# Kernel tuning notes

Measured on AMD Instinct MI355X. Metric: run time of the kernel, lower is better.

The kernel has to match this reference:

```python
import jax, jax.numpy as jnp
import numpy as np

# ---- config (matches init_kwargs + VMamba/MambaIR SS2D defaults) ----
B, LEN, C, H, W = 2, 3, 64, 64, 64
N_STATE = 16           # d_state
D_INNER = 2 * C        # expand=2
DT_RANK = C // 16      # ceil(d_model/16)
K = 4                  # 4 scan directions
EPS = 1e-5


def _ln_last(x, g, b):
    m = x.mean(-1, keepdims=True)
    v = x.var(-1, keepdims=True)
    return (x - m) * jax.lax.rsqrt(v + EPS) * g + b


def _instance_ln(x):
    # kalman.utils.layer_norm: normalize each sample over (C,H,W), no affine
    m = x.mean(axis=(1, 2, 3), keepdims=True)
    v = x.var(axis=(1, 2, 3), keepdims=True)
    return (x - m) * jax.lax.rsqrt(v + EPS)


def _gn(x, g, b):
    # GroupNorm with num_groups=1 on NCHW
    m = x.mean(axis=(1, 2, 3), keepdims=True)
    v = x.var(axis=(1, 2, 3), keepdims=True)
    return (x - m) * jax.lax.rsqrt(v + EPS) * g[None, :, None, None] + b[None, :, None, None]


def _conv2d(x, w, b, groups=1):
    y = jax.lax.conv_general_dilated(x, w, (1, 1), 'SAME',
            dimension_numbers=('NCHW', 'OIHW', 'NCHW'), feature_group_count=groups)
    return y + b[None, :, None, None]


def _selective_scan(xs, dts, Bs, Cs, A, Ds, dt_bias):
    # xs, dts: (Bt,K,D,L); Bs, Cs: (Bt,K,N,L); A: (K,D,N); Ds, dt_bias: (K,D)
    delta = jax.nn.softplus(dts + dt_bias[None, :, :, None])
    u_t = jnp.moveaxis(xs, -1, 0)      # (L,Bt,K,D)
    d_t = jnp.moveaxis(delta, -1, 0)
    B_t = jnp.moveaxis(Bs, -1, 0)      # (L,Bt,K,N)
    C_t = jnp.moveaxis(Cs, -1, 0)
    h0 = jnp.zeros((xs.shape[0], K, xs.shape[2], A.shape[-1]), xs.dtype)

    def step(h, inp):
        u, d, Bv, Cv = inp
        dA = jnp.exp(d[..., None] * A)                                  # (Bt,K,D,N)
        h = dA * h + d[..., None] * Bv[:, :, None, :] * u[..., None]
        y = jnp.einsum('bkdn,bkn->bkd', h, Cv)
        return h, y

    _, ys = jax.lax.scan(step, h0, (u_t, d_t, B_t, C_t))
    ys = jnp.moveaxis(ys, 0, -1)                                        # (Bt,K,D,L)
    return ys + xs * Ds[None, :, :, None]


def _ss2d(x, in_proj_w, dwconv_w, dwconv_b, x_proj_w, dt_proj_w, dt_proj_b,
          A_logs, Ds, out_norm_g, out_norm_b, out_proj_w):
    Bt, Hh, Ww, Cc = x.shape
    L = Hh * Ww
    xz = x @ in_proj_w.T                               # (Bt,H,W,2*Di)
    xx, z = jnp.split(xz, 2, axis=-1)
    xx = jnp.transpose(xx, (0, 3, 1, 2))               # (Bt,Di,H,W)
    xx = jax.nn.silu(_conv2d(xx, dwconv_w, dwconv_b, groups=D_INNER))
    hw = xx.reshape(Bt, D_INNER, L)
    wh = jnp.transpose(xx, (0, 1, 3, 2)).reshape(Bt, D_INNER, L)
    xs = jnp.stack([hw, wh, hw[..., ::-1], wh[..., ::-1]], axis=1)      # (Bt,4,Di,L)
    x_dbl = jnp.einsum('bkdl,kcd->bkcl', xs, x_proj_w)
    dts = jnp.einsum('bkrl,kdr->bkdl', x_dbl[:, :, :DT_RANK], dt_proj_w)
    Bs = x_dbl[:, :, DT_RANK:DT_RANK + N_STATE]
    Cs = x_dbl[:, :, DT_RANK + N_STATE:]
    A = -jnp.exp(A_logs)                               # (K,Di,N)
    out_y = _selective_scan(xs, dts, Bs, Cs, A, Ds, dt_proj_b)
    inv = out_y[:, 2:4, :, ::-1]

    def wh2hw(y):
        return jnp.transpose(y.reshape(Bt, D_INNER, Ww, Hh), (0, 1, 3, 2)).reshape(Bt, D_INNER, L)

    y = out_y[:, 0] + inv[:, 0] + wh2hw(out_y[:, 1]) + wh2hw(inv[:, 1])
    y = jnp.transpose(y.reshape(Bt, D_INNER, Hh, Ww), (0, 2, 3, 1))
    y = _ln_last(y, out_norm_g, out_norm_b)
    y = y * jax.nn.silu(z)
    return y @ out_proj_w.T


def setup_inputs() -> dict:
    key = jax.random.key(0)
    ks = jax.random.split(key, 16)
    rn = lambda k, s, sc=0.05: jax.random.normal(k, s, jnp.float32) * sc
    inp = {}
    inp['image_sequence'] = jax.random.normal(ks[0], (B, LEN, C, H, W), jnp.float32)
    inp['difficult_zone'] = jax.random.normal(ks[1], (B, C, H, W), jnp.float32)
    inp['sigma'] = jax.random.uniform(ks[2], (B, C, H, W), jnp.float32)
    inp['gn1_g'] = jnp.ones((3 * C,)); inp['gn1_b'] = jnp.zeros((3 * C,))
    inp['conv1_w'] = rn(ks[3], (C, 3 * C, 3, 3)); inp['conv1_b'] = jnp.zeros((C,))
    inp['gn2_g'] = jnp.ones((C,)); inp['gn2_b'] = jnp.zeros((C,))
    inp['conv2_w'] = rn(ks[4], (C, C, 3, 3)); inp['conv2_b'] = jnp.zeros((C,))
    inp['skip_w'] = rn(ks[5], (C, 3 * C, 1, 1)); inp['skip_b'] = jnp.zeros((C,))
    inp['ln1_g'] = jnp.ones((C,)); inp['ln1_b'] = jnp.zeros((C,))
    inp['ln2_g'] = jnp.ones((C,)); inp['ln2_b'] = jnp.zeros((C,))
    inp['in_proj_w'] = rn(ks[6], (2 * D_INNER, C))
    inp['dwconv_w'] = rn(ks[7], (D_INNER, 1, 3, 3)); inp['dwconv_b'] = jnp.zeros((D_INNER,))
    inp['x_proj_w'] = rn(ks[8], (K, DT_RANK + 2 * N_STATE, D_INNER))
    inp['dt_proj_w'] = rn(ks[9], (K, D_INNER, DT_RANK), 0.2)
    inp['dt_proj_b'] = rn(ks[10], (K, D_INNER), 0.1)
    inp['A_logs'] = jnp.log(jnp.broadcast_to(jnp.arange(1, N_STATE + 1, dtype=jnp.float32), (K, D_INNER, N_STATE)))
    inp['Ds'] = jnp.ones((K, D_INNER))
    inp['out_norm_g'] = jnp.ones((D_INNER,)); inp['out_norm_b'] = jnp.zeros((D_INNER,))
    inp['out_proj_w'] = rn(ks[11], (C, D_INNER))
    inp['fc1_w'] = rn(ks[12], (C, C)); inp['fc1_b'] = jnp.zeros((C,))
    inp['fc2_w'] = rn(ks[13], (C, C)); inp['fc2_b'] = jnp.zeros((C,))
    return inp


def reference(image_sequence, difficult_zone, sigma,
              gn1_g, gn1_b, conv1_w, conv1_b, gn2_g, gn2_b, conv2_w, conv2_b, skip_w, skip_b,
              ln1_g, ln1_b, ln2_g, ln2_b,
              in_proj_w, dwconv_w, dwconv_b, x_proj_w, dt_proj_w, dt_proj_b,
              A_logs, Ds, out_norm_g, out_norm_b, out_proj_w,
              fc1_w, fc1_b, fc2_w, fc2_b):
    Bsz, Lf, Cc, Hh, Ww = image_sequence.shape
    # per-frame layer_norm; frames are independent so fold them into batch
    img = _instance_ln(image_sequence.reshape(Bsz * Lf, Cc, Hh, Ww)).reshape(Bsz, Lf, Cc, Hh, Ww)
    dz = jnp.broadcast_to(difficult_zone[:, None], (Bsz, Lf, Cc, Hh, Ww))
    sg = jnp.broadcast_to(sigma[:, None], (Bsz, Lf, Cc, Hh, Ww))
    x = jnp.concatenate([dz, img, sg], axis=2).reshape(Bsz * Lf, 3 * Cc, Hh, Ww)
    # ConvolutionalResBlock (GN -> SiLU -> conv, x2, + 1x1 skip)
    h = _conv2d(jax.nn.silu(_gn(x, gn1_g, gn1_b)), conv1_w, conv1_b)
    h = _conv2d(jax.nn.silu(_gn(h, gn2_g, gn2_b)), conv2_w, conv2_b)
    x = h + _conv2d(x, skip_w, skip_b)
    # VSSBlock (pre-norm): x + SS2D(LN(x)); x + Mlp(LN(x))
    x = jnp.transpose(x, (0, 2, 3, 1))                 # NHWC
    x = x + _ss2d(_ln_last(x, ln1_g, ln1_b), in_proj_w, dwconv_w, dwconv_b,
                  x_proj_w, dt_proj_w, dt_proj_b, A_logs, Ds,
                  out_norm_g, out_norm_b, out_proj_w)
    xm = _ln_last(x, ln2_g, ln2_b)
    x = x + (jax.nn.gelu(xm @ fc1_w.T + fc1_b) @ fc2_w.T + fc2_b)
    x = jnp.transpose(x, (0, 3, 1, 2)).reshape(Bsz, Lf, Cc, Hh, Ww)
    return x
```

## Files before the change

kernel.cpp:

```cpp
#include <hip/hip_runtime.h>
#include <hip/hip_bf16.h>

typedef unsigned short ushortT;
typedef short short8v __attribute__((ext_vector_type(8)));
typedef float float4v __attribute__((ext_vector_type(4)));

#define NBL 6
#define NC 64
#define NC3 192
#define NHW 4096
#define NDI 128
#define NNS 16
#define NDR 4
#define NK 4
#define NL 4096
#define NCH 128
#define SCLEN 32
#define NSTATE 49152

static const size_t F_XCAT  = 0;
static const size_t F_ACT1  = 4718592;
static const size_t F_H1    = 9437184;
static const size_t F_ACT2  = 11010048;
static const size_t F_H2    = 12582912;
static const size_t F_XRES  = 14155776;
static const size_t F_XXIN  = 15728640;
static const size_t F_Z     = 18874368;
static const size_t F_XXC   = 22020096;
static const size_t F_XDBL  = 25165824;
static const size_t F_YS    = 28704768;
static const size_t F_YCOMB = 41287680;
static const size_t F_X1    = 44433408;
static const size_t F_X2    = 46006272;
static const size_t F_STATS = 47579136;
static const size_t F_TOTAL = 47579184;

__device__ __forceinline__ float wred64(float v) {
#pragma unroll
  for (int m = 32; m; m >>= 1) v += __shfl_xor(v, m, 64);
  return v;
}

__device__ __forceinline__ float silu(float v) {
  return v / (1.f + __expf(-v));
}

__device__ __forceinline__ ushortT f2bf(float f) {
  unsigned int u = __builtin_bit_cast(unsigned int, f);
  unsigned int r = (u + 0x7FFFu + ((u >> 16) & 1u)) >> 16;
  return (ushortT)r;
}

__device__ __forceinline__ int map_pos(int k, int l) {
  if (k == 0) return l;
  if (k == 1) return ((l & 63) << 6) | (l >> 6);
  if (k == 2) return 4095 - l;
  int lp = 4095 - l;
  return ((lp & 63) << 6) | (lp >> 6);
}

__device__ __forceinline__ float softplus_fast(float a) {
  float t = exp2f(a * 1.44269504f);
  float r = 0.69314718f * __log2f(1.f + t);
  return (a > 20.f) ? a : r;
}

__device__ __forceinline__ void pow_tree(float E1, float4v& e0, float4v& e1,
                                         float4v& e2, float4v& e3) {
  float E2 = E1 * E1, E3 = E2 * E1, E4 = E2 * E2;
  float E5 = E4 * E1, E6 = E4 * E2, E7 = E4 * E3, E8 = E4 * E4;
  e0[0] = E1; e0[1] = E2; e0[2] = E3; e0[3] = E4;
  e1[0] = E5; e1[1] = E6; e1[2] = E7; e1[3] = E8;
  e2[0] = E8 * E1; e2[1] = E8 * E2; e2[2] = E8 * E3; e2[3] = E8 * E4;
  e3[0] = E8 * E5; e3[1] = E8 * E6; e3[2] = E8 * E7; e3[3] = E8 * E8;
}

__global__ __launch_bounds__(256) void wtrans_kernel(const float* __restrict__ src,
                                                     float* __restrict__ dst, int O, int C) {
  int id = blockIdx.x * 256 + threadIdx.x;
  if (id >= O * C) return;
  int c = id / O, o = id % O;
  dst[id] = src[o * C + c];
}

__global__ __launch_bounds__(256) void stats1_kernel(const float* __restrict__ in, int n,
                                                     double* __restrict__ part) {
  int bi = blockIdx.x;
  int s = bi >> 5, j = bi & 31;
  int slice = n >> 5;
  const float4* p = (const float4*)(in + (size_t)s * n + (size_t)j * slice);
  int n4 = slice >> 2;
  double dsum = 0.0, dsq = 0.0;
  for (int i = threadIdx.x; i < n4; i += 256) {
    float4 v = p[i];
    dsum += (double)((v.x + v.y) + (v.z + v.w));
    dsq += (double)v.x * v.x + (double)v.y * v.y + (double)v.z * v.z + (double)v.w * v.w;
  }
  __shared__ double s1[256], s2[256];
  s1[threadIdx.x] = dsum; s2[threadIdx.x] = dsq;
  __syncthreads();
  for (int off = 128; off; off >>= 1) {
    if (threadIdx.x < off) { s1[threadIdx.x] += s1[threadIdx.x + off]; s2[threadIdx.x] += s2[threadIdx.x + off]; }
    __syncthreads();
  }
  if (threadIdx.x == 0) { part[2 * bi] = s1[0]; part[2 * bi + 1] = s2[0]; }
}

__global__ __launch_bounds__(64) void stats2_kernel(const double* __restrict__ part, int n,
                                                    float* __restrict__ mean_out,
                                                    float* __restrict__ rstd_out) {
  int s = blockIdx.x;
  int lane = threadIdx.x;
  double sum = 0.0, sq = 0.0;
  if (lane < 32) { sum = part[2 * (s * 32 + lane)]; sq = part[2 * (s * 32 + lane) + 1]; }
#pragma unroll
  for (int m = 16; m; m >>= 1) { sum += __shfl_xor(sum, m, 64); sq += __shfl_xor(sq, m, 64); }
  if (lane == 0) {
    double mean = sum / n;
    double var = sq / n - mean * mean;
    mean_out[s] = (float)mean;
    rstd_out[s] = (float)(1.0 / sqrt(var + 1e-5));
  }
}

__global__ __launch_bounds__(256) void build_xcat_kernel(const float* __restrict__ img,
                                                         const float* __restrict__ dz,
                                                         const float* __restrict__ sg,
                                                         const float* __restrict__ stats,
                                                         float* __restrict__ xcat) {
  size_t gid = (size_t)blockIdx.x * 256 + threadIdx.x;
  int p = gid & 4095;
  size_t r = gid >> 12;
  int ch = (int)(r % NC3);
  int bl = (int)(r / NC3);
  int b = bl / 3;
  float v;
  if (ch < 64) {
    v = dz[((size_t)b * NC + ch) * NHW + p];
  } else if (ch < 128) {
    float m = stats[bl], rs = stats[8 + bl];
    v = (img[((size_t)bl * NC + (ch - 64)) * NHW + p] - m) * rs;
  } else {
    v = sg[((size_t)b * NC + (ch - 128)) * NHW + p];
  }
  xcat[gid] = v;
}

template <int CCH>
__global__ __launch_bounds__(256) void gnsilu_t_kernel(const float* __restrict__ in,
                                                       const float* __restrict__ g,
                                                       const float* __restrict__ b,
                                                       const float* __restrict__ stats,
                                                       ushortT* __restrict__ outb) {
  int bi = blockIdx.x;
  int bl = bi >> 6, h = bi & 63;
  __shared__ ushortT tile[CCH][66];
  float m = stats[bl], rs = stats[8 + bl];
  int t = threadIdx.x;
  for (int idx = t; idx < CCH * 64; idx += 256) {
    int ch = idx >> 6, w = idx & 63;
    float v = in[(((size_t)bl * CCH + ch) << 12) + (h << 6) + w];
    v = (v - m) * rs * g[ch] + b[ch];
    v = silu(v);
    tile[ch][w] = f2bf(v);
  }
  __syncthreads();
  constexpr int C8 = CCH / 8;
  for (int idx = t; idx < 64 * C8; idx += 256) {
    int w = idx / C8, c8 = idx % C8;
    short8v v;
#pragma unroll
    for (int j = 0; j < 8; ++j) v[j] = (short)tile[c8 * 8 + j][w];
    *(short8v*)&outb[(size_t)(bl * 4096 + h * 64 + w) * CCH + c8 * 8] = v;
  }
}

__global__ __launch_bounds__(256) void wprep_kernel(const float* __restrict__ w,
                                                    ushortT* __restrict__ out,
                                                    int CIN, int KT) {
  int id = blockIdx.x * 256 + threadIdx.x;
  int j = id & 7;
  int lane = (id >> 3) & 63;
  int nt = (id >> 9) & 3;
  int rest = id >> 11;
  int kt = rest % KT;
  int tap = rest / KT;
  int oc = nt * 16 + (lane & 15);
  int ic = kt * 32 + ((lane >> 4) << 3) + j;
  int r = tap / 3, s = tap % 3;
  out[id] = f2bf(w[(((size_t)oc * CIN + ic) * 3 + r) * 3 + s]);
}

template <int CIN>
__global__ __launch_bounds__(256) void conv_mfma_kernel(const ushortT* __restrict__ actb,
                                                        const ushortT* __restrict__ wb,
                                                        const float* __restrict__ bias,
                                                        float* __restrict__ out) {
  constexpr int KT = CIN / 32;
  constexpr int STRIDE = CIN + 8;
  constexpr int C8 = CIN / 8;
  int bi = blockIdx.x;
  int nh = bi & 1;
  int h = (bi >> 1) & 63;
  int bl = bi >> 7;
  int t = threadIdx.x;
  int wv = t >> 6, lane = t & 63;
  __shared__ ushortT lds[66 * STRIDE];
  float4v acc0 = {0.f, 0.f, 0.f, 0.f};
  float4v acc1 = {0.f, 0.f, 0.f, 0.f};
  int lrow = lane & 15;
  int lk = (lane >> 4) << 3;
  for (int dy = 0; dy < 3; ++dy) {
    int hh = h + dy - 1;
    bool valid = (hh >= 0) && (hh < 64);
    int hc = valid ? hh : 0;
    if (dy) __syncthreads();
    const ushortT* src = actb + (size_t)(bl * 4096 + hc * 64) * CIN;
    for (int idx = t; idx < 64 * C8; idx += 256) {
      int w = idx / C8, c8 = idx % C8;
      short8v v = {0, 0, 0, 0, 0, 0, 0, 0};
      if (valid) v = *(const short8v*)&src[(size_t)w * CIN + c8 * 8];
      *(short8v*)&lds[(w + 1) * STRIDE + c8 * 8] = v;
    }
    if (t < 2 * C8) {
      int which = t / C8, c8 = t % C8;
      short8v z = {0, 0, 0, 0, 0, 0, 0, 0};
      *(short8v*)&lds[(which ? 65 : 0) * STRIDE + c8 * 8] = z;
    }
    __syncthreads();
    for (int dx = 0; dx < 3; ++dx) {
      int tap = dy * 3 + dx;
      int wl = (wv << 4) + lrow + dx;
#pragma unroll
      for (int kt = 0; kt < KT; ++kt) {
        short8v a = *(const short8v*)&lds[wl * STRIDE + kt * 32 + lk];
        const ushortT* wp = wb + ((size_t)(((tap * KT + kt) * 4 + (nh << 1)) * 64 + lane) << 3);
        short8v b0 = *(const short8v*)&wp[0];
        short8v b1 = *(const short8v*)&wp[512];
        acc0 = __builtin_amdgcn_mfma_f32_16x16x32_bf16(a, b0, acc0, 0, 0, 0);
        acc1 = __builtin_amdgcn_mfma_f32_16x16x32_bf16(a, b1, acc1, 0, 0, 0);
      }
    }
  }
  int oc0 = (nh << 5) + lrow;
  int oc1 = oc0 + 16;
  int w0 = (wv << 4) + ((lane >> 4) << 2);
  float bv0 = bias[oc0], bv1 = bias[oc1];
  float4 o0 = make_float4(acc0[0] + bv0, acc0[1] + bv0, acc0[2] + bv0, acc0[3] + bv0);
  float4 o1 = make_float4(acc1[0] + bv1, acc1[1] + bv1, acc1[2] + bv1, acc1[3] + bv1);
  *(float4*)&out[(((size_t)bl * 64 + oc0) << 12) + (h << 6) + w0] = o0;
  *(float4*)&out[(((size_t)bl * 64 + oc1) << 12) + (h << 6) + w0] = o1;
}

__global__ __launch_bounds__(256) void skip_kernel(const float* __restrict__ xcat,
                                                   const float* __restrict__ h2,
                                                   const float* __restrict__ skwt,
                                                   const float* __restrict__ skb,
                                                   float* __restrict__ xres) {
  int bi = blockIdx.x;
  int bl = bi >> 6, h = bi & 63;
  int t = threadIdx.x;
  int oc = t & 63, w0 = (t >> 6) << 4;
  __shared__ float lds[64][64];
  float acc[16];
#pragma unroll
  for (int i = 0; i < 16; ++i) acc[i] = 0.f;
  for (int cc = 0; cc < 3; ++cc) {
    __syncthreads();
    for (int idx = t; idx < 4096; idx += 256) {
      int ch = idx >> 6, w = idx & 63;
      lds[ch][w] = xcat[(((size_t)bl * NC3 + cc * 64 + ch) << 12) + (h << 6) + w];
    }
    __syncthreads();
    for (int ch = 0; ch < 64; ++ch) {
      float wv = skwt[((cc << 6) + ch) * 64 + oc];
#pragma unroll
      for (int i = 0; i < 16; ++i) acc[i] += wv * lds[ch][w0 + i];
    }
  }
  float bv = skb[oc];
  int p0 = (h << 6) + w0;
#pragma unroll
  for (int i = 0; i < 16; ++i) {
    float hv = h2[(((size_t)bl * 64 + oc) << 12) + p0 + i];
    xres[((size_t)bl * NHW + p0 + i) * 64 + oc] = acc[i] + bv + hv;
  }
}

__global__ __launch_bounds__(256) void inproj_kernel(const float* __restrict__ xres,
                                                     const float* __restrict__ g,
                                                     const float* __restrict__ b,
                                                     const float* __restrict__ wt,
                                                     float* __restrict__ xxin,
                                                     float* __restrict__ z) {
  int wv = threadIdx.x >> 6, lane = threadIdx.x & 63;
  size_t pi0 = (size_t)blockIdx.x << 4;
  __shared__ float xb[64][16];
  float gv = g[lane], bv = b[lane];
#pragma unroll
  for (int j = 0; j < 4; ++j) {
    int p = (wv << 2) + j;
    float x = xres[(pi0 + p) * 64 + lane];
    float s = wred64(x);
    float s2 = wred64(x * x);
    float m = s * (1.f / 64), var = s2 * (1.f / 64) - m * m;
    float rstd = rsqrtf(var + 1e-5f);
    xb[lane][p] = (x - m) * rstd * gv + bv;
  }
  __syncthreads();
  int oc = (wv << 6) + lane;
  float4v a0 = {0.f, 0.f, 0.f, 0.f}, a1 = a0, a2 = a0, a3 = a0;
  for (int c = 0; c < 64; ++c) {
    float w = wt[(c << 8) + oc];
    const float4v* xr = (const float4v*)&xb[c][0];
    a0 += w * xr[0];
    a1 += w * xr[1];
    a2 += w * xr[2];
    a3 += w * xr[3];
  }
  float acc[16];
  *(float4v*)&acc[0] = a0;
  *(float4v*)&acc[4] = a1;
  *(float4v*)&acc[8] = a2;
  *(float4v*)&acc[12] = a3;
  float* dst = (oc < 128) ? xxin : z;
  int oco = (oc < 128) ? oc : (oc - 128);
#pragma unroll
  for (int p = 0; p < 16; ++p) dst[((pi0 + p) << 7) + oco] = acc[p];
}

__global__ __launch_bounds__(256) void dwconv_kernel(const float* __restrict__ xx,
                                                     const float* __restrict__ w,
                                                     const float* __restrict__ b,
                                                     float* __restrict__ out) {
  size_t gid = (size_t)blockIdx.x * 256 + threadIdx.x;
  int d = gid & 127;
  size_t pi = gid >> 7;
  int p = (int)(pi & 4095);
  int bl = (int)(pi >> 12);
  int h = p >> 6, wq = p & 63;
  float acc = b[d];
  const float* wr = w + d * 9;
#pragma unroll
  for (int dy = -1; dy <= 1; ++dy) {
    int hh = h + dy;
    if (hh < 0 || hh >= 64) continue;
#pragma unroll
    for (int dx = -1; dx <= 1; ++dx) {
      int ww = wq + dx;
      if (ww < 0 || ww >= 64) continue;
      acc += wr[(dy + 1) * 3 + (dx + 1)] * xx[(((size_t)bl << 12) + (hh << 6) + ww) * 128 + d];
    }
  }
  out[pi * 128 + d] = silu(acc);
}

__global__ __launch_bounds__(256) void xdbl_kernel(const float* __restrict__ xxc,
                                                   const float* __restrict__ xpw,
                                                   float* __restrict__ xdbl) {
  int bi = blockIdx.x;
  int lt = bi & 63;
  int korder = (bi >> 6) & 1;
  int bl = bi >> 7;
  int lbase = lt << 6;
  __shared__ float xs[64 * 128];
  int t = threadIdx.x;
#pragma unroll
  for (int it = 0; it < 8; ++it) {
    int idx = it * 256 + t;
    int i = idx >> 5, d4 = idx & 31;
    int l = lbase + i;
    int pos = korder ? (((l & 63) << 6) | (l >> 6)) : l;
    float4 v = *(const float4*)&xxc[((size_t)bl * NHW + pos) * 128 + (d4 << 2)];
    int slot = d4 ^ (i & 7);
    *(float4*)&xs[i * 128 + (slot << 2)] = v;
  }
  __syncthreads();
  int wv = __builtin_amdgcn_readfirstlane(t >> 6);
  int lane = t & 63;
  int k_w = korder + ((wv >= 2) ? 2 : 0);
  int c0 = (wv & 1) * 18;
  float acc[18];
#pragma unroll
  for (int j = 0; j < 18; ++j) acc[j] = 0.f;
  const float* wbase = xpw + (size_t)(k_w * 36 + c0) * 128;
  for (int d4 = 0; d4 < 32; ++d4) {
    int slot = d4 ^ (lane & 7);
    float4 x4 = *(const float4*)&xs[lane * 128 + (slot << 2)];
#pragma unroll
    for (int j = 0; j < 18; ++j) {
      float4 w4 = *(const float4*)&wbase[j * 128 + (d4 << 2)];
      acc[j] += w4.x * x4.x + w4.y * x4.y + w4.z * x4.z + w4.w * x4.w;
    }
  }
  int lout = (k_w < 2) ? (lbase + lane) : (4095 - lbase - lane);
  size_t obase = ((size_t)(bl * 4 + k_w) * 36 + c0) * (size_t)NL + lout;
#pragma unroll
  for (int j = 0; j < 18; ++j)
    xdbl[obase + (size_t)j * NL] = acc[j];
}

__global__ __launch_bounds__(128) void scan_pass1_kernel(const float* __restrict__ xdbl,
                                                         const float* __restrict__ xxc,
                                                         const float* __restrict__ dtw,
                                                         const float* __restrict__ dtb,
                                                         const float* __restrict__ Alog,
                                                         float* __restrict__ chunkP,
                                                         float* __restrict__ chunkH) {
  int bi = blockIdx.x;
  int chunk = bi & (NCH - 1);
  int bk = bi >> 7;
  int k = bk & 3, bl = bk >> 2;
  int d = threadIdx.x;
  float4 wv = *(const float4*)(dtw + (size_t)(((k << 7) + d) << 2));
  float bias = dtb[(k << 7) + d];
  const float* ar = Alog + (size_t)(((k << 7) + d) << 4);
  float a1v = -__expf(ar[0]) * 1.44269504f;
  bool geom = true;
#pragma unroll
  for (int n = 1; n < 16; ++n) {
    float an = -__expf(ar[n]) * 1.44269504f;
    geom = geom && (fabsf(an - (float)(n + 1) * a1v) <= 1e-3f * fabsf((float)(n + 1) * a1v) + 1e-6f);
  }
  __shared__ float xd[SCLEN][20];
  int l0 = chunk << 5;
  for (int idx = threadIdx.x; idx < 20 * SCLEN; idx += 128) {
    int c = idx >> 5, li = idx & 31;
    xd[li][c] = xdbl[((size_t)bk * 36 + c) * (size_t)NL + l0 + li];
  }
  __syncthreads();
  const float* uB = xxc + ((size_t)bl << 19) + d;
  float4v h0 = {0.f, 0.f, 0.f, 0.f}, h1 = h0, h2 = h0, h3 = h0;
  float sdt = 0.f;
  float u_nxt = uB[(size_t)map_pos(k, l0) << 7];
  if (geom) {
    for (int li = 0; li < SCLEN; ++li) {
      float u = u_nxt;
      int nl = (li < SCLEN - 1) ? (li + 1) : (SCLEN - 1);
      u_nxt = uB[(size_t)map_pos(k, l0 + nl) << 7];
      const float4v* row = (const float4v*)&xd[li][0];
      float4v q0 = row[0];
      float accq = bias + wv.x * q0[0] + wv.y * q0[1] + wv.z * q0[2] + wv.w * q0[3];
      float dt = softplus_fast(accq);
      float dtu = dt * u;
      sdt += dt;
      float4v b0 = row[1], b1 = row[2], b2 = row[3], b3 = row[4];
      float4v e0, e1, e2, e3;
      pow_tree(exp2f(a1v * dt), e0, e1, e2, e3);
      h0 = e0 * h0 + dtu * b0;
      h1 = e1 * h1 + dtu * b1;
      h2 = e2 * h2 + dtu * b2;
      h3 = e3 * h3 + dtu * b3;
    }
  } else {
    float4v a0v, a1q, a2q, a3q;
#pragma unroll
    for (int j = 0; j < 4; ++j) {
      a0v[j] = -__expf(ar[j]) * 1.44269504f;
      a1q[j] = -__expf(ar[4 + j]) * 1.44269504f;
      a2q[j] = -__expf(ar[8 + j]) * 1.44269504f;
      a3q[j] = -__expf(ar[12 + j]) * 1.44269504f;
    }
    for (int li = 0; li < SCLEN; ++li) {
      float u = u_nxt;
      int nl = (li < SCLEN - 1) ? (li + 1) : (SCLEN - 1);
      u_nxt = uB[(size_t)map_pos(k, l0 + nl) << 7];
      const float4v* row = (const float4v*)&xd[li][0];
      float4v q0 = row[0];
      float accq = bias + wv.x * q0[0] + wv.y * q0[1] + wv.z * q0[2] + wv.w * q0[3];
      float dt = softplus_fast(accq);
      float dtu = dt * u;
      sdt += dt;
      float4v b0 = row[1], b1 = row[2], b2 = row[3], b3 = row[4];
      float4v e0, e1, e2, e3;
#pragma unroll
      for (int j = 0; j < 4; ++j) {
        e0[j] = exp2f(a0v[j] * dt);
        e1[j] = exp2f(a1q[j] * dt);
        e2[j] = exp2f(a2q[j] * dt);
        e3[j] = exp2f(a3q[j] * dt);
      }
      h0 = e0 * h0 + dtu * b0;
      h1 = e1 * h1 + dtu * b1;
      h2 = e2 * h2 + dtu * b2;
      h3 = e3 * h3 + dtu * b3;
    }
  }
  size_t base = (size_t)chunk * NSTATE + (((size_t)bk << 7) + (size_t)d) * 16;
  float4v p0, p1, p2, p3;
  if (geom) {
    pow_tree(exp2f(a1v * sdt), p0, p1, p2, p3);
  } else {
#pragma unroll
    for (int j = 0; j < 4; ++j) {
      p0[j] = exp2f(-__expf(ar[j]) * 1.44269504f * sdt);
      p1[j] = exp2f(-__expf(ar[4 + j]) * 1.44269504f * sdt);
      p2[j] = exp2f(-__expf(ar[8 + j]) * 1.44269504f * sdt);
      p3[j] = exp2f(-__expf(ar[12 + j]) * 1.44269504f * sdt);
    }
  }
  *(float4v*)&chunkP[base + 0] = p0;
  *(float4v*)&chunkP[base + 4] = p1;
  *(float4v*)&chunkP[base + 8] = p2;
  *(float4v*)&chunkP[base + 12] = p3;
  *(float4v*)&chunkH[base + 0] = h0;
  *(float4v*)&chunkH[base + 4] = h1;
  *(float4v*)&chunkH[base + 8] = h2;
  *(float4v*)&chunkH[base + 12] = h3;
}

__global__ __launch_bounds__(256) void scan_pass2_kernel(const float* __restrict__ chunkP,
                                                         const float* __restrict__ chunkH,
                                                         float* __restrict__ chunkHS) {
  size_t state = (size_t)blockIdx.x * 256 + threadIdx.x;
  float h = 0.f;
#pragma unroll 4
  for (int j = 0; j < NCH; ++j) {
    size_t idx = (size_t)j * NSTATE + state;
    chunkHS[idx] = h;
    h = chunkP[idx] * h + chunkH[idx];
  }
}

__global__ __launch_bounds__(128) void scan_pass3_kernel(const float* __restrict__ xdbl,
                                                         const float* __restrict__ xxc,
                                                         const float* __restrict__ dtw,
                                                         const float* __restrict__ dtb,
                                                         const float* __restrict__ Alog,
                                                         const float* __restrict__ chunkHS,
                                                         float* __restrict__ ys) {
  int bi = blockIdx.x;
  int chunk = bi & (NCH - 1);
  int bk = bi >> 7;
  int k = bk & 3, bl = bk >> 2;
  int d = threadIdx.x;
  float4 wv = *(const float4*)(dtw + (size_t)(((k << 7) + d) << 2));
  float bias = dtb[(k << 7) + d];
  const float* ar = Alog + (size_t)(((k << 7) + d) << 4);
  float a1v = -__expf(ar[0]) * 1.44269504f;
  bool geom = true;
#pragma unroll
  for (int n = 1; n < 16; ++n) {
    float an = -__expf(ar[n]) * 1.44269504f;
    geom = geom && (fabsf(an - (float)(n + 1) * a1v) <= 1e-3f * fabsf((float)(n + 1) * a1v) + 1e-6f);
  }
  __shared__ float xd[SCLEN][36];
  int l0 = chunk << 5;
  for (int idx = threadIdx.x; idx < 36 * SCLEN; idx += 128) {
    int c = idx >> 5, li = idx & 31;
    xd[li][c] = xdbl[((size_t)bk * 36 + c) * (size_t)NL + l0 + li];
  }
  __syncthreads();
  const float* uB = xxc + ((size_t)bl << 19) + d;
  float* yB = ys + ((size_t)bk << 19) + d;
  size_t base = (size_t)chunk * NSTATE + (((size_t)bk << 7) + (size_t)d) * 16;
  float4v h0 = *(const float4v*)&chunkHS[base + 0];
  float4v h1 = *(const float4v*)&chunkHS[base + 4];
  float4v h2 = *(const float4v*)&chunkHS[base + 8];
  float4v h3 = *(const float4v*)&chunkHS[base + 12];
  float u_nxt = uB[(size_t)map_pos(k, l0) << 7];
  if (geom) {
    for (int li = 0; li < SCLEN; ++li) {
      float u = u_nxt;
      int nl = (li < SCLEN - 1) ? (li + 1) : (SCLEN - 1);
      u_nxt = uB[(size_t)map_pos(k, l0 + nl) << 7];
      const float4v* row = (const float4v*)&xd[li][0];
      float4v q0 = row[0];
      float accq = bias + wv.x * q0[0] + wv.y * q0[1] + wv.z * q0[2] + wv.w * q0[3];
      float dt = softplus_fast(accq);
      float dtu = dt * u;
      float4v b0 = row[1], b1 = row[2], b2 = row[3], b3 = row[4];
      float4v c0 = row[5], c1 = row[6], c2 = row[7], c3 = row[8];
      float4v e0, e1, e2, e3;
      pow_tree(exp2f(a1v * dt), e0, e1, e2, e3);
      h0 = e0 * h0 + dtu * b0;
      h1 = e1 * h1 + dtu * b1;
      h2 = e2 * h2 + dtu * b2;
      h3 = e3 * h3 + dtu * b3;
      float4v sy = h0 * c0;
      sy += h1 * c1;
      sy += h2 * c2;
      sy += h3 * c3;
      yB[(size_t)(l0 + li) << 7] = (sy[0] + sy[1]) + (sy[2] + sy[3]);
    }
  } else {
    float4v a0v, a1q, a2q, a3q;
#pragma unroll
    for (int j = 0; j < 4; ++j) {
      a0v[j] = -__expf(ar[j]) * 1.44269504f;
      a1q[j] = -__expf(ar[4 + j]) * 1.44269504f;
      a2q[j] = -__expf(ar[8 + j]) * 1.44269504f;
      a3q[j] = -__expf(ar[12 + j]) * 1.44269504f;
    }
    for (int li = 0; li < SCLEN; ++li) {
      float u = u_nxt;
      int nl = (li < SCLEN - 1) ? (li + 1) : (SCLEN - 1);
      u_nxt = uB[(size_t)map_pos(k, l0 + nl) << 7];
      const float4v* row = (const float4v*)&xd[li][0];
      float4v q0 = row[0];
      float accq = bias + wv.x * q0[0] + wv.y * q0[1] + wv.z * q0[2] + wv.w * q0[3];
      float dt = softplus_fast(accq);
      float dtu = dt * u;
      float4v b0 = row[1], b1 = row[2], b2 = row[3], b3 = row[4];
      float4v c0 = row[5], c1 = row[6], c2 = row[7], c3 = row[8];
      float4v e0, e1, e2, e3;
#pragma unroll
      for (int j = 0; j < 4; ++j) {
        e0[j] = exp2f(a0v[j] * dt);
        e1[j] = exp2f(a1q[j] * dt);
        e2[j] = exp2f(a2q[j] * dt);
        e3[j] = exp2f(a3q[j] * dt);
      }
      h0 = e0 * h0 + dtu * b0;
      h1 = e1 * h1 + dtu * b1;
      h2 = e2 * h2 + dtu * b2;
      h3 = e3 * h3 + dtu * b3;
      float4v sy = h0 * c0;
      sy += h1 * c1;
      sy += h2 * c2;
      sy += h3 * c3;
      yB[(size_t)(l0 + li) << 7] = (sy[0] + sy[1]) + (sy[2] + sy[3]);
    }
  }
}

__global__ __launch_bounds__(256) void combine_kernel(const float* __restrict__ ys,
                                                      const float* __restrict__ xxc,
                                                      const float* __restrict__ Ds,
                                                      float* __restrict__ ycomb) {
  size_t gid = (size_t)blockIdx.x * 256 + threadIdx.x;
  int d = gid & 127;
  size_t pi = gid >> 7;
  int p = (int)(pi & 4095);
  int bl = (int)(pi >> 12);
  int h = p >> 6, w = p & 63;
  int l1 = (w << 6) | h;
  size_t base = ((size_t)bl * 4) << 12;
  float v = ys[((base + p) << 7) + d]
          + ys[((base + 4096 + l1) << 7) + d]
          + ys[((base + 2 * 4096 + (4095 - p)) << 7) + d]
          + ys[((base + 3 * 4096 + (4095 - l1)) << 7) + d];
  float ds = Ds[d] + Ds[128 + d] + Ds[256 + d] + Ds[384 + d];
  v += xxc[(pi << 7) + d] * ds;
  ycomb[(pi << 7) + d] = v;
}

__global__ __launch_bounds__(256) void outproj_kernel(const float* __restrict__ ycomb,
                                                      const float* __restrict__ z,
                                                      const float* __restrict__ ong,
                                                      const float* __restrict__ onb,
                                                      const float* __restrict__ opwt,
                                                      const float* __restrict__ xres,
                                                      float* __restrict__ x1) {
  int wv = threadIdx.x >> 6, lane = threadIdx.x & 63;
  size_t pi0 = (size_t)blockIdx.x << 4;
  __shared__ float gb[128][16];
  float og0 = ong[lane], ob0 = onb[lane];
  float og1 = ong[64 + lane], ob1 = onb[64 + lane];
#pragma unroll
  for (int j = 0; j < 4; ++j) {
    int p = (wv << 2) + j;
    size_t pp = pi0 + p;
    float y0 = ycomb[(pp << 7) + lane], y1 = ycomb[(pp << 7) + 64 + lane];
    float s = wred64(y0 + y1);
    float s2 = wred64(y0 * y0 + y1 * y1);
    float m = s * (1.f / 128), var = s2 * (1.f / 128) - m * m;
    float rstd = rsqrtf(var + 1e-5f);
    float z0 = z[(pp << 7) + lane], z1 = z[(pp << 7) + 64 + lane];
    gb[lane][p] = ((y0 - m) * rstd * og0 + ob0) * silu(z0);
    gb[64 + lane][p] = ((y1 - m) * rstd * og1 + ob1) * silu(z1);
  }
  __syncthreads();
  int p0 = wv << 2;
  float4v acc = {0.f, 0.f, 0.f, 0.f};
  for (int c = 0; c < 128; ++c) {
    float w = opwt[(c << 6) + lane];
    acc += w * (*(const float4v*)&gb[c][p0]);
  }
  float accs[4];
  *(float4v*)&accs[0] = acc;
#pragma unroll
  for (int j = 0; j < 4; ++j) {
    size_t pp = pi0 + p0 + j;
    x1[pp * 64 + lane] = xres[pp * 64 + lane] + accs[j];
  }
}

__global__ __launch_bounds__(256) void mlp_kernel(const float* __restrict__ x1,
                                                  const float* __restrict__ g2,
                                                  const float* __restrict__ b2,
                                                  const float* __restrict__ w1t,
                                                  const float* __restrict__ bb1,
                                                  const float* __restrict__ w2t,
                                                  const float* __restrict__ bb2,
                                                  float* __restrict__ x2) {
  int wv = threadIdx.x >> 6, lane = threadIdx.x & 63;
  size_t pi0 = (size_t)blockIdx.x << 4;
  __shared__ float xb[64][16], tb[64][16];
  float gv = g2[lane], bv = b2[lane];
  float xsave[4];
#pragma unroll
  for (int j = 0; j < 4; ++j) {
    int p = (wv << 2) + j;
    float xv = x1[(pi0 + p) * 64 + lane];
    xsave[j] = xv;
    float s = wred64(xv), s2 = wred64(xv * xv);
    float m = s * (1.f / 64), var = s2 * (1.f / 64) - m * m;
    float rstd = rsqrtf(var + 1e-5f);
    xb[lane][p] = (xv - m) * rstd * gv + bv;
  }
  __syncthreads();
  int p0 = wv << 2;
  float bb1v = bb1[lane];
  float4v acc = {bb1v, bb1v, bb1v, bb1v};
  for (int c = 0; c < 64; ++c) {
    float w = w1t[(c << 6) + lane];
    acc += w * (*(const float4v*)&xb[c][p0]);
  }
  float us[4];
  *(float4v*)&us[0] = acc;
#pragma unroll
  for (int j = 0; j < 4; ++j) {
    float u = us[j];
    float tt = tanhf(0.7978845608028654f * (u + 0.044715f * u * u * u));
    tb[lane][p0 + j] = 0.5f * u * (1.f + tt);
  }
  __syncthreads();
  float bb2v = bb2[lane];
  float4v acc2 = {bb2v, bb2v, bb2v, bb2v};
  for (int c = 0; c < 64; ++c) {
    float w = w2t[(c << 6) + lane];
    acc2 += w * (*(const float4v*)&tb[c][p0]);
  }
  float o2[4];
  *(float4v*)&o2[0] = acc2;
#pragma unroll
  for (int j = 0; j < 4; ++j)
    x2[(pi0 + p0 + j) * 64 + lane] = xsave[j] + o2[j];
}

__global__ __launch_bounds__(256) void transpose_out_kernel(const float* __restrict__ x2,
                                                            float* __restrict__ out) {
  int bi = blockIdx.x;
  int pt = bi & 127;
  int ct = (bi >> 7) & 1;
  int bl = bi >> 8;
  __shared__ float lds[32][33];
  int t = threadIdx.x;
  int j = t & 31, i0 = t >> 5;
  int p0 = pt << 5, c0 = ct << 5;
#pragma unroll
  for (int q = 0; q < 4; ++q) {
    int i = i0 + (q << 3);
    lds[i][j] = x2[((size_t)bl * NHW + p0 + i) * 64 + c0 + j];
  }
  __syncthreads();
#pragma unroll
  for (int q = 0; q < 4; ++q) {
    int i = i0 + (q << 3);
    out[((size_t)bl * 64 + c0 + i) * (size_t)NHW + p0 + j] = lds[j][i];
  }
}

extern "C" void kernel_launch(void* const* d_in, const int* in_sizes, int n_in,
                              void* d_out, int out_size, void* d_ws, size_t ws_size,
                              hipStream_t stream) {
  const float* img  = (const float*)d_in[0];
  const float* dz   = (const float*)d_in[1];
  const float* sg   = (const float*)d_in[2];
  const float* gn1g = (const float*)d_in[3];
  const float* gn1b = (const float*)d_in[4];
  const float* c1w  = (const float*)d_in[5];
  const float* c1b  = (const float*)d_in[6];
  const float* gn2g = (const float*)d_in[7];
  const float* gn2b = (const float*)d_in[8];
  const float* c2w  = (const float*)d_in[9];
  const float* c2b  = (const float*)d_in[10];
  const float* skw  = (const float*)d_in[11];
  const float* skb  = (const float*)d_in[12];
  const float* ln1g = (const float*)d_in[13];
  const float* ln1b = (const float*)d_in[14];
  const float* ln2g = (const float*)d_in[15];
  const float* ln2b = (const float*)d_in[16];
  const float* ipw  = (const float*)d_in[17];
  const float* dww  = (const float*)d_in[18];
  const float* dwb  = (const float*)d_in[19];
  const float* xpw  = (const float*)d_in[20];
  const float* dtw  = (const float*)d_in[21];
  const float* dtb  = (const float*)d_in[22];
  const float* Alog = (const float*)d_in[23];
  const float* Dsp  = (const float*)d_in[24];
  const float* ong  = (const float*)d_in[25];
  const float* onb  = (const float*)d_in[26];
  const float* opw  = (const float*)d_in[27];
  const float* f1w  = (const float*)d_in[28];
  const float* f1b  = (const float*)d_in[29];
  const float* f2w  = (const float*)d_in[30];
  const float* f2b  = (const float*)d_in[31];

  float* out = (float*)d_out;
  float* ws = (float*)d_ws;
  if (ws_size < F_TOTAL * sizeof(float)) return;

  float* xcat  = ws + F_XCAT;
  float* h1    = ws + F_H1;
  float* h2    = ws + F_H2;
  float* xres  = ws + F_XRES;
  float* xxin  = ws + F_XXIN;
  float* zbuf  = ws + F_Z;
  float* xxc   = ws + F_XXC;
  float* xdbl  = ws + F_XDBL;
  float* ysb   = ws + F_YS;
  float* ycomb = ws + F_YCOMB;
  float* x1    = ws + F_X1;
  float* x2    = ws + F_X2;
  float* stats = ws + F_STATS;
  ushortT* act1b = (ushortT*)(ws + F_ACT1);
  ushortT* act2b = (ushortT*)(ws + F_ACT2);
  double* part  = (double*)(ws + F_X2);
  ushortT* wb1  = (ushortT*)(ws + F_X2 + 1024);
  ushortT* wb2  = wb1 + 110592;
  float* chunkP  = ws + F_YS;
  float* chunkH  = ws + F_YS + 6291456;
  float* chunkHS = ws + F_XCAT;
  float* wt_sk = ws + F_ACT1;
  float* wt_ip = ws + F_XCAT;
  float* wt_op = ws + F_XXIN;
  float* wt_f1 = ws + F_XXIN + 8192;
  float* wt_f2 = ws + F_XXIN + 12288;

  wprep_kernel<<<432, 256, 0, stream>>>(c1w, wb1, NC3, 6);
  wprep_kernel<<<144, 256, 0, stream>>>(c2w, wb2, NC, 2);
  stats1_kernel<<<NBL * 32, 256, 0, stream>>>(img, NC * NHW, part);
  stats2_kernel<<<NBL, 64, 0, stream>>>(part, NC * NHW, stats + 0, stats + 8);
  build_xcat_kernel<<<18432, 256, 0, stream>>>(img, dz, sg, stats, xcat);
  stats1_kernel<<<NBL * 32, 256, 0, stream>>>(xcat, NC3 * NHW, part);
  stats2_kernel<<<NBL, 64, 0, stream>>>(part, NC3 * NHW, stats + 16, stats + 24);
  gnsilu_t_kernel<NC3><<<NBL * 64, 256, 0, stream>>>(xcat, gn1g, gn1b, stats + 16, act1b);
  conv_mfma_kernel<NC3><<<NBL * 64 * 2, 256, 0, stream>>>(act1b, wb1, c1b, h1);
  wtrans_kernel<<<48, 256, 0, stream>>>(skw, wt_sk, 64, 192);
  stats1_kernel<<<NBL * 32, 256, 0, stream>>>(h1, NC * NHW, part);
  stats2_kernel<<<NBL, 64, 0, stream>>>(part, NC * NHW, stats + 32, stats + 40);
  gnsilu_t_kernel<NC><<<NBL * 64, 256, 0, stream>>>(h1, gn2g, gn2b, stats + 32, act2b);
  conv_mfma_kernel<NC><<<NBL * 64 * 2, 256, 0, stream>>>(act2b, wb2, c2b, h2);
  skip_kernel<<<NBL * 64, 256, 0, stream>>>(xcat, h2, wt_sk, skb, xres);
  wtrans_kernel<<<64, 256, 0, stream>>>(ipw, wt_ip, 256, 64);
  inproj_kernel<<<1536, 256, 0, stream>>>(xres, ln1g, ln1b, wt_ip, xxin, zbuf);
  dwconv_kernel<<<12288, 256, 0, stream>>>(xxin, dww, dwb, xxc);
  wtrans_kernel<<<32, 256, 0, stream>>>(opw, wt_op, 64, 128);
  wtrans_kernel<<<16, 256, 0, stream>>>(f1w, wt_f1, 64, 64);
  wtrans_kernel<<<16, 256, 0, stream>>>(f2w, wt_f2, 64, 64);
  xdbl_kernel<<<NBL * 2 * 64, 256, 0, stream>>>(xxc, xpw, xdbl);
  scan_pass1_kernel<<<24 * NCH, 128, 0, stream>>>(xdbl, xxc, dtw, dtb, Alog, chunkP, chunkH);
  scan_pass2_kernel<<<192, 256, 0, stream>>>(chunkP, chunkH, chunkHS);
  scan_pass3_kernel<<<24 * NCH, 128, 0, stream>>>(xdbl, xxc, dtw, dtb, Alog, chunkHS, ysb);
  combine_kernel<<<12288, 256, 0, stream>>>(ysb, xxc, Dsp, ycomb);
  outproj_kernel<<<1536, 256, 0, stream>>>(ycomb, zbuf, ong, onb, wt_op, xres, x1);
  mlp_kernel<<<1536, 256, 0, stream>>>(x1, ln2g, ln2b, wt_f1, f1b, wt_f2, f2b, x2);
  transpose_out_kernel<<<NBL * 256, 256, 0, stream>>>(x2, out);
}
```

Before: 355.1 us.

## Store per-chunk dt sums instead of decay products and fuse combine into outproj

Scan pass 1 now writes one summed dt per chunk and channel instead of 16 per-state decay factors. Pass 2 recomputes each decay with exp2f from A_log and that sum, which cuts the chunkP write and read traffic. The four-direction combine plus the D skip term moves into the out-projection kernel, removing the ycomb intermediate and one launch. The cost is extra exp work in the serial pass-2 loop, and the 4-way gather now sits inside outproj.

```diff
diff --git a/kernel.cpp b/kernel.cpp
--- a/kernel.cpp
+++ b/kernel.cpp
@@ -405,7 +405,7 @@
                                                          const float* __restrict__ dtw,
                                                          const float* __restrict__ dtb,
                                                          const float* __restrict__ Alog,
-                                                         float* __restrict__ chunkP,
+                                                         float* __restrict__ chunkSdt,
                                                          float* __restrict__ chunkH) {
   int bi = blockIdx.x;
   int chunk = bi & (NCH - 1);
@@ -487,38 +487,26 @@
     }
   }
   size_t base = (size_t)chunk * NSTATE + (((size_t)bk << 7) + (size_t)d) * 16;
-  float4v p0, p1, p2, p3;
-  if (geom) {
-    pow_tree(exp2f(a1v * sdt), p0, p1, p2, p3);
-  } else {
-#pragma unroll
-    for (int j = 0; j < 4; ++j) {
-      p0[j] = exp2f(-__expf(ar[j]) * 1.44269504f * sdt);
-      p1[j] = exp2f(-__expf(ar[4 + j]) * 1.44269504f * sdt);
-      p2[j] = exp2f(-__expf(ar[8 + j]) * 1.44269504f * sdt);
-      p3[j] = exp2f(-__expf(ar[12 + j]) * 1.44269504f * sdt);
-    }
-  }
-  *(float4v*)&chunkP[base + 0] = p0;
-  *(float4v*)&chunkP[base + 4] = p1;
-  *(float4v*)&chunkP[base + 8] = p2;
-  *(float4v*)&chunkP[base + 12] = p3;
+  chunkSdt[(size_t)chunk * 3072 + (bk << 7) + d] = sdt;
   *(float4v*)&chunkH[base + 0] = h0;
   *(float4v*)&chunkH[base + 4] = h1;
   *(float4v*)&chunkH[base + 8] = h2;
   *(float4v*)&chunkH[base + 12] = h3;
 }
 
-__global__ __launch_bounds__(256) void scan_pass2_kernel(const float* __restrict__ chunkP,
+__global__ __launch_bounds__(256) void scan_pass2_kernel(const float* __restrict__ chunkSdt,
                                                          const float* __restrict__ chunkH,
+                                                         const float* __restrict__ Alog,
                                                          float* __restrict__ chunkHS) {
   size_t state = (size_t)blockIdx.x * 256 + threadIdx.x;
+  float an = -__expf(Alog[state & 8191]) * 1.44269504f;
+  int kd = (int)(state >> 4);
   float h = 0.f;
-#pragma unroll 4
   for (int j = 0; j < NCH; ++j) {
     size_t idx = (size_t)j * NSTATE + state;
     chunkHS[idx] = h;
-    h = chunkP[idx] * h + chunkH[idx];
+    float sdt = chunkSdt[(size_t)j * 3072 + kd];
+    h = exp2f(an * sdt) * h + chunkH[idx];
   }
 }
 
@@ -624,28 +612,9 @@
   }
 }
 
-__global__ __launch_bounds__(256) void combine_kernel(const float* __restrict__ ys,
+__global__ __launch_bounds__(256) void outproj_kernel(const float* __restrict__ ys,
                                                       const float* __restrict__ xxc,
                                                       const float* __restrict__ Ds,
-                                                      float* __restrict__ ycomb) {
-  size_t gid = (size_t)blockIdx.x * 256 + threadIdx.x;
-  int d = gid & 127;
-  size_t pi = gid >> 7;
-  int p = (int)(pi & 4095);
-  int bl = (int)(pi >> 12);
-  int h = p >> 6, w = p & 63;
-  int l1 = (w << 6) | h;
-  size_t base = ((size_t)bl * 4) << 12;
-  float v = ys[((base + p) << 7) + d]
-          + ys[((base + 4096 + l1) << 7) + d]
-          + ys[((base + 2 * 4096 + (4095 - p)) << 7) + d]
-          + ys[((base + 3 * 4096 + (4095 - l1)) << 7) + d];
-  float ds = Ds[d] + Ds[128 + d] + Ds[256 + d] + Ds[384 + d];
-  v += xxc[(pi << 7) + d] * ds;
-  ycomb[(pi << 7) + d] = v;
-}
-
-__global__ __launch_bounds__(256) void outproj_kernel(const float* __restrict__ ycomb,
                                                       const float* __restrict__ z,
                                                       const float* __restrict__ ong,
                                                       const float* __restrict__ onb,
@@ -657,11 +626,24 @@
   __shared__ float gb[128][16];
   float og0 = ong[lane], ob0 = onb[lane];
   float og1 = ong[64 + lane], ob1 = onb[64 + lane];
+  float ds0 = Ds[lane] + Ds[128 + lane] + Ds[256 + lane] + Ds[384 + lane];
+  float ds1 = Ds[64 + lane] + Ds[192 + lane] + Ds[320 + lane] + Ds[448 + lane];
 #pragma unroll
   for (int j = 0; j < 4; ++j) {
     int p = (wv << 2) + j;
     size_t pp = pi0 + p;
-    float y0 = ycomb[(pp << 7) + lane], y1 = ycomb[(pp << 7) + 64 + lane];
+    int bl = (int)(pp >> 12);
+    int pg = (int)(pp & 4095);
+    int h = pg >> 6, w = pg & 63;
+    int l1 = (w << 6) | h;
+    size_t base = ((size_t)bl * 4) << 12;
+    size_t i0 = (base + pg) << 7;
+    size_t i1 = (base + 4096 + l1) << 7;
+    size_t i2 = (base + 2 * 4096 + (4095 - pg)) << 7;
+    size_t i3 = (base + 3 * 4096 + (4095 - l1)) << 7;
+    float xx0 = xxc[(pp << 7) + lane], xx1 = xxc[(pp << 7) + 64 + lane];
+    float y0 = ys[i0 + lane] + ys[i1 + lane] + ys[i2 + lane] + ys[i3 + lane] + xx0 * ds0;
+    float y1 = ys[i0 + 64 + lane] + ys[i1 + 64 + lane] + ys[i2 + 64 + lane] + ys[i3 + 64 + lane] + xx1 * ds1;
     float s = wred64(y0 + y1);
     float s2 = wred64(y0 * y0 + y1 * y1);
     float m = s * (1.f / 128), var = s2 * (1.f / 128) - m * m;
@@ -811,7 +793,6 @@
   float* xxc   = ws + F_XXC;
   float* xdbl  = ws + F_XDBL;
   float* ysb   = ws + F_YS;
-  float* ycomb = ws + F_YCOMB;
   float* x1    = ws + F_X1;
   float* x2    = ws + F_X2;
   float* stats = ws + F_STATS;
@@ -820,9 +801,9 @@
   double* part  = (double*)(ws + F_X2);
   ushortT* wb1  = (ushortT*)(ws + F_X2 + 1024);
   ushortT* wb2  = wb1 + 110592;
-  float* chunkP  = ws + F_YS;
-  float* chunkH  = ws + F_YS + 6291456;
-  float* chunkHS = ws + F_XCAT;
+  float* chunkH   = ws + F_YS;
+  float* chunkSdt = ws + F_YS + 6291456;
+  float* chunkHS  = ws + F_XCAT;
   float* wt_sk = ws + F_ACT1;
   float* wt_ip = ws + F_XCAT;
   float* wt_op = ws + F_XXIN;
@@ -851,11 +832,10 @@
   wtrans_kernel<<<16, 256, 0, stream>>>(f1w, wt_f1, 64, 64);
   wtrans_kernel<<<16, 256, 0, stream>>>(f2w, wt_f2, 64, 64);
   xdbl_kernel<<<NBL * 2 * 64, 256, 0, stream>>>(xxc, xpw, xdbl);
-  scan_pass1_kernel<<<24 * NCH, 128, 0, stream>>>(xdbl, xxc, dtw, dtb, Alog, chunkP, chunkH);
-  scan_pass2_kernel<<<192, 256, 0, stream>>>(chunkP, chunkH, chunkHS);
+  scan_pass1_kernel<<<24 * NCH, 128, 0, stream>>>(xdbl, xxc, dtw, dtb, Alog, chunkSdt, chunkH);
+  scan_pass2_kernel<<<192, 256, 0, stream>>>(chunkSdt, chunkH, Alog, chunkHS);
   scan_pass3_kernel<<<24 * NCH, 128, 0, stream>>>(xdbl, xxc, dtw, dtb, Alog, chunkHS, ysb);
-  combine_kernel<<<12288, 256, 0, stream>>>(ysb, xxc, Dsp, ycomb);
-  outproj_kernel<<<1536, 256, 0, stream>>>(ycomb, zbuf, ong, onb, wt_op, xres, x1);
+  outproj_kernel<<<1536, 256, 0, stream>>>(ysb, xxc, Dsp, zbuf, ong, onb, wt_op, xres, x1);
   mlp_kernel<<<1536, 256, 0, stream>>>(x1, ln2g, ln2b, wt_f1, f1b, wt_f2, f2b, x2);
   transpose_out_kernel<<<NBL * 256, 256, 0, stream>>>(x2, out);
 }
```

Measured after the change: 358.8 us. Within noise of the previous version (+1.1%).
